# Kernel optimization log

Measured on AMD Instinct MI355X. Metric: run time of the kernel, lower is better.

## Reference

```python
import jax, jax.numpy as jnp
import numpy as np

POOL_NUM = 1024
NEIGHBOR_NUM = 16


def setup_inputs() -> dict:
    key = jax.random.key(0)
    k1, k2 = jax.random.split(key)
    vertices = jax.random.normal(k1, (8, 4096, 3), dtype=jnp.float32)
    feature_map = jax.random.normal(k2, (8, 4096, 256), dtype=jnp.float32)
    return {"vertices": vertices, "feature_map": feature_map}


def _get_neighbor_index(vertices, neighbor_num):
    # vertices: (bs, N, 3) -> neighbor_index: (bs, N, neighbor_num)
    inner = jnp.einsum('bnd,bmd->bnm', vertices, vertices)  # (bs, N, N)
    quadratic = jnp.sum(vertices ** 2, axis=2)              # (bs, N)
    distance = -2.0 * inner + quadratic[:, None, :] + quadratic[:, :, None]
    # smallest k+1 distances -> top_k on negated distance
    _, idx = jax.lax.top_k(-distance, neighbor_num + 1)     # (bs, N, k+1)
    return idx[:, :, 1:]                                    # drop self


def reference(vertices, feature_map):
    bs, vertice_num, _ = vertices.shape
    neighbor_index = _get_neighbor_index(vertices, NEIGHBOR_NUM)  # (bs, N, k)
    # gather neighbor features: (bs, N, k, C)
    id_0 = jnp.arange(bs)[:, None, None]
    neighbor_feature = feature_map[id_0, neighbor_index]
    pooled_feature = jnp.max(neighbor_feature, axis=2)            # (bs, N, C)
    # deterministic random subsample of vertices (torch uses randperm)
    sample_idx = jax.random.permutation(jax.random.key(42), vertice_num)[:POOL_NUM]
    vertices_pool = vertices[:, sample_idx, :]                    # (bs, P, 3)
    feature_map_pool = pooled_feature[:, sample_idx, :]           # (bs, P, C)
    return (vertices_pool, feature_map_pool)
```

## Files before the change

kernel.cpp:

```cpp
#include <hip/hip_runtime.h>
#include <stdint.h>
#include <string.h>
#include <algorithm>

#define NV 4096
#define NPOOL 1024
#define NB 8
#define KNB 16
#define REMOVED 0xFFFFFFFFu
#define HIDX(b) ((((b) >> 4) | (((b) & 15) << 6)))

struct SIdx { unsigned short v[NPOOL]; };

static inline void tf2x32_host(uint32_t k0, uint32_t k1,
                               uint32_t c0, uint32_t c1,
                               uint32_t& o0, uint32_t& o1) {
  uint32_t ks0 = k0, ks1 = k1, ks2 = k0 ^ k1 ^ 0x1BD11BDAu;
  uint32_t x0 = c0 + ks0, x1 = c1 + ks1;
#define TFR(r) { x0 += x1; x1 = (x1 << (r)) | (x1 >> (32 - (r))); x1 ^= x0; }
  TFR(13) TFR(15) TFR(26) TFR(6)
  x0 += ks1; x1 += ks2 + 1u;
  TFR(17) TFR(29) TFR(16) TFR(24)
  x0 += ks2; x1 += ks0 + 2u;
  TFR(13) TFR(15) TFR(26) TFR(6)
  x0 += ks0; x1 += ks1 + 3u;
  TFR(17) TFR(29) TFR(16) TFR(24)
  x0 += ks1; x1 += ks2 + 4u;
  TFR(13) TFR(15) TFR(26) TFR(6)
  x0 += ks2; x1 += ks0 + 5u;
#undef TFR
  o0 = x0; o1 = x1;
}

static void compute_sample_idx(SIdx& out) {
  static_assert(sizeof(SIdx) == 2048, "kernarg size");
  uint64_t arr[NV];
  uint16_t x[NV], tmp[NV];
  for (int i = 0; i < NV; ++i) x[i] = (uint16_t)i;
  uint32_t kh = 0u, kl = 42u;
  for (int round = 0; round < 2; ++round) {
    uint32_t nkh, nkl, sh, sl, t0, t1;
    tf2x32_host(kh, kl, 0u, 0u, nkh, nkl);
    tf2x32_host(kh, kl, 0u, 1u, sh, sl);
    kh = nkh; kl = nkl;
    for (int i = 0; i < NV; ++i) {
      tf2x32_host(sh, sl, 0u, (uint32_t)i, t0, t1);
      arr[i] = ((uint64_t)(t0 ^ t1) << 32) | (uint32_t)i;
    }
    std::sort(arr, arr + NV);
    for (int i = 0; i < NV; ++i) tmp[i] = x[(uint32_t)(arr[i] & 0xffffffffu)];
    memcpy(x, tmp, sizeof(x));
  }
  for (int i = 0; i < NPOOL; ++i) out.v[i] = x[i];
}

__global__ __launch_bounds__(256) void knn_pool_kernel(
    const float* __restrict__ vertices, const float* __restrict__ fm,
    const SIdx sidx,
    float* __restrict__ outV, float* __restrict__ outF) {
  __shared__ uint32_t hist[1024];
  __shared__ unsigned long long cand[64];
  __shared__ unsigned long long wmin[4];
  __shared__ int winners[KNB];
  __shared__ int s_ncand, s_taub;

  const int tid = threadIdx.x;
  const int lane = tid & 63;
  const int warp = tid >> 6;
  const int q = blockIdx.x;
  const int b = q & 7;
  const int i = q >> 3;
  const int n = (int)sidx.v[i];

  const float* vb = vertices + (size_t)b * NV * 3;
  const float qx = vb[n * 3 + 0], qy = vb[n * 3 + 1], qz = vb[n * 3 + 2];
  const float qn = __fadd_rn(__fadd_rn(__fmul_rn(qx, qx), __fmul_rn(qy, qy)),
                             __fmul_rn(qz, qz));

  const float4* vb4 = (const float4*)vb + tid * 12;
  float f[48];
#pragma unroll
  for (int j = 0; j < 12; ++j) {
    const float4 v4 = vb4[j];
    f[4 * j + 0] = v4.x; f[4 * j + 1] = v4.y;
    f[4 * j + 2] = v4.z; f[4 * j + 3] = v4.w;
  }

  uint32_t d[16];
#pragma unroll
  for (int t = 0; t < 16; ++t) {
    const int m = (tid << 4) + t;
    const float cx = f[3 * t + 0], cy = f[3 * t + 1], cz = f[3 * t + 2];
    const float inner = __fmaf_rn(cz, qz, __fmaf_rn(cy, qy, __fmul_rn(cx, qx)));
    const float qm = __fadd_rn(__fadd_rn(__fmul_rn(cx, cx), __fmul_rn(cy, cy)),
                               __fmul_rn(cz, cz));
    const float dist = __fadd_rn(__fadd_rn(__fmul_rn(-2.0f, inner), qm), qn);
    d[t] = (m == n) ? REMOVED : __float_as_uint(dist);
  }

  uint32_t mn = d[0];
#pragma unroll
  for (int t = 1; t < 16; ++t) mn = (d[t] < mn) ? d[t] : mn;

  hist[tid] = 0; hist[tid + 256] = 0; hist[tid + 512] = 0; hist[tid + 768] = 0;
  if (tid == 0) s_ncand = 0;
  __syncthreads();

  atomicAdd(&hist[HIDX(mn >> 22)], 1u);
  __syncthreads();

  if (warp == 0) {
    uint32_t s = 0;
#pragma unroll
    for (int j = 0; j < 16; ++j) s += hist[j * 64 + lane];
    uint32_t inc = s;
    for (int off = 1; off < 64; off <<= 1) {
      const uint32_t o = (uint32_t)__shfl_up((int)inc, off);
      if (lane >= off) inc += o;
    }
    const uint32_t pre = inc - s;
    const bool cross = (pre < KNB) && (inc >= KNB);
    const unsigned long long bal = __ballot(cross);
    const int leader = __ffsll((unsigned long long)bal) - 1;
    if (lane == leader) {
      uint32_t c = pre;
      int tb = lane * 16 + 15;
      for (int j = 0; j < 16; ++j) {
        const uint32_t h = hist[j * 64 + lane];
        if (c + h >= KNB) { tb = lane * 16 + j; break; }
        c += h;
      }
      s_taub = tb;
    }
  }
  __syncthreads();

  const uint32_t taub = (uint32_t)s_taub;

#pragma unroll
  for (int t = 0; t < 16; ++t) {
    const uint32_t v = d[t];
    if ((v >> 22) <= taub) {
      const int s = atomicAdd(&s_ncand, 1);
      if (s < 64)
        cand[s] = ((unsigned long long)v << 32) | (uint32_t)((tid << 4) + t);
    }
  }
  __syncthreads();

  const int C = s_ncand;
  if (C <= 64) {
    if (warp == 0) {
      const unsigned long long me =
          (lane < C) ? cand[lane] : 0xFFFFFFFFFFFFFFFFull;
      int rank = 0;
      for (int j = 0; j < C; ++j)
        rank += (cand[j] < me) ? 1 : 0;
      if (lane < C && rank < KNB) winners[rank] = (int)(me & 0xFFFFFFFFu);
    }
    __syncthreads();
  } else {
    uint32_t mask = 0;
    for (int r = 0; r < KNB; ++r) {
      uint32_t bv = REMOVED, bm = 0xFFFFFFFFu;
#pragma unroll
      for (int t = 0; t < 16; ++t) {
        const uint32_t v = (((mask >> t) & 1u) || ((d[t] >> 22) > taub))
                               ? REMOVED : d[t];
        const uint32_t m = (uint32_t)((tid << 4) + t);
        if (v < bv || (v == bv && m < bm)) { bv = v; bm = m; }
      }
      for (int off = 32; off > 0; off >>= 1) {
        const uint32_t ov = (uint32_t)__shfl_down((int)bv, off);
        const uint32_t om = (uint32_t)__shfl_down((int)bm, off);
        if (ov < bv || (ov == bv && om < bm)) { bv = ov; bm = om; }
      }
      if (lane == 0) wmin[warp] = ((unsigned long long)bv << 32) | bm;
      __syncthreads();
      const unsigned long long p0 = wmin[0], p1 = wmin[1];
      const unsigned long long p2 = wmin[2], p3 = wmin[3];
      const unsigned long long pa = (p0 < p1) ? p0 : p1;
      const unsigned long long pb = (p2 < p3) ? p2 : p3;
      const int w = (int)(((pa < pb) ? pa : pb) & 0xFFFFFFFFu);
      if (tid == 0) winners[r] = w;
      if (tid == (w >> 4)) mask |= 1u << (w & 15);
      __syncthreads();
    }
  }

  const float* fmb = fm + (size_t)b * NV * 256;
  float af = -INFINITY;
#pragma unroll
  for (int s = 0; s < KNB; ++s) {
    const int w = winners[s];
    af = fmaxf(af, fmb[(size_t)w * 256 + tid]);
  }
  outF[((size_t)b * NPOOL + i) * 256 + tid] = af;

  if (tid < 3) {
    outV[((size_t)b * NPOOL + i) * 3 + tid] = vb[n * 3 + tid];
  }
}

extern "C" void kernel_launch(void* const* d_in, const int* in_sizes, int n_in,
                              void* d_out, int out_size, void* d_ws, size_t ws_size,
                              hipStream_t stream) {
  const float* vertices = (const float*)d_in[0];
  const float* fm = (const float*)d_in[1];
  float* out = (float*)d_out;
  float* outV = out;
  float* outF = out + NB * NPOOL * 3;

  SIdx sidx;
  compute_sample_idx(sidx);

  knn_pool_kernel<<<NB * NPOOL, 256, 0, stream>>>(vertices, fm, sidx, outV, outF);
}
```

Measured before the change: 40.96 us.

## Process two query points per block to reuse loaded candidate vertices

Each block now handles two sampled query vertices instead of one, so the 4096 candidate coordinates loaded into registers serve two distance computations. Histograms, candidate lists and winner arrays are duplicated, and the two selection passes run in separate warps. The feature max-gather is vectorized with float4 loads over two warps. The grid is halved, which reduces parallelism and adds register pressure from keeping two distance arrays live.

```diff
diff --git a/kernel.cpp b/kernel.cpp
--- a/kernel.cpp
+++ b/kernel.cpp
@@ -54,28 +54,63 @@
   for (int i = 0; i < NPOOL; ++i) out.v[i] = x[i];
 }
 
+#define FALLBACK(D, TAUB, WIN)                                             \
+  {                                                                        \
+    uint32_t mask = 0;                                                     \
+    for (int r = 0; r < KNB; ++r) {                                        \
+      uint32_t bv = REMOVED, bm = 0xFFFFFFFFu;                             \
+      _Pragma("unroll")                                                    \
+      for (int t = 0; t < 16; ++t) {                                       \
+        const uint32_t v = (((mask >> t) & 1u) || ((D[t] >> 22) > (TAUB))) \
+                               ? REMOVED : D[t];                           \
+        const uint32_t m = (uint32_t)((tid << 4) + t);                     \
+        if (v < bv || (v == bv && m < bm)) { bv = v; bm = m; }             \
+      }                                                                    \
+      for (int off = 32; off > 0; off >>= 1) {                             \
+        const uint32_t ov = (uint32_t)__shfl_down((int)bv, off);           \
+        const uint32_t om = (uint32_t)__shfl_down((int)bm, off);           \
+        if (ov < bv || (ov == bv && om < bm)) { bv = ov; bm = om; }        \
+      }                                                                    \
+      if (lane == 0) wmin[warp] = ((unsigned long long)bv << 32) | bm;     \
+      __syncthreads();                                                     \
+      const unsigned long long p0 = wmin[0], p1 = wmin[1];                 \
+      const unsigned long long p2 = wmin[2], p3 = wmin[3];                 \
+      const unsigned long long pa = (p0 < p1) ? p0 : p1;                   \
+      const unsigned long long pb = (p2 < p3) ? p2 : p3;                   \
+      const int w = (int)(((pa < pb) ? pa : pb) & 0xFFFFFFFFu);            \
+      if (tid == 0) (WIN)[r] = w;                                          \
+      if (tid == (w >> 4)) mask |= 1u << (w & 15);                         \
+      __syncthreads();                                                     \
+    }                                                                      \
+  }
+
 __global__ __launch_bounds__(256) void knn_pool_kernel(
     const float* __restrict__ vertices, const float* __restrict__ fm,
     const SIdx sidx,
     float* __restrict__ outV, float* __restrict__ outF) {
-  __shared__ uint32_t hist[1024];
-  __shared__ unsigned long long cand[64];
+  __shared__ uint32_t hist0[1024], hist1[1024];
+  __shared__ unsigned long long cand0[64], cand1[64];
   __shared__ unsigned long long wmin[4];
-  __shared__ int winners[KNB];
-  __shared__ int s_ncand, s_taub;
+  __shared__ int winners0[KNB], winners1[KNB];
+  __shared__ int s_nc0, s_nc1, s_tb0, s_tb1;
 
   const int tid = threadIdx.x;
   const int lane = tid & 63;
   const int warp = tid >> 6;
-  const int q = blockIdx.x;
-  const int b = q & 7;
-  const int i = q >> 3;
-  const int n = (int)sidx.v[i];
+  const int blk = blockIdx.x;
+  const int b = blk & 7;
+  const int i0 = (blk >> 3) << 1;
+  const int i1 = i0 | 1;
+  const int n0 = (int)sidx.v[i0];
+  const int n1 = (int)sidx.v[i1];
 
   const float* vb = vertices + (size_t)b * NV * 3;
-  const float qx = vb[n * 3 + 0], qy = vb[n * 3 + 1], qz = vb[n * 3 + 2];
-  const float qn = __fadd_rn(__fadd_rn(__fmul_rn(qx, qx), __fmul_rn(qy, qy)),
-                             __fmul_rn(qz, qz));
+  const float q0x = vb[n0 * 3 + 0], q0y = vb[n0 * 3 + 1], q0z = vb[n0 * 3 + 2];
+  const float q1x = vb[n1 * 3 + 0], q1y = vb[n1 * 3 + 1], q1z = vb[n1 * 3 + 2];
+  const float qn0 = __fadd_rn(__fadd_rn(__fmul_rn(q0x, q0x), __fmul_rn(q0y, q0y)),
+                              __fmul_rn(q0z, q0z));
+  const float qn1 = __fadd_rn(__fadd_rn(__fmul_rn(q1x, q1x), __fmul_rn(q1y, q1y)),
+                              __fmul_rn(q1z, q1z));
 
   const float4* vb4 = (const float4*)vb + tid * 12;
   float f[48];
@@ -86,33 +121,43 @@
     f[4 * j + 2] = v4.z; f[4 * j + 3] = v4.w;
   }
 
-  uint32_t d[16];
+  uint32_t d0[16], d1[16];
 #pragma unroll
   for (int t = 0; t < 16; ++t) {
     const int m = (tid << 4) + t;
     const float cx = f[3 * t + 0], cy = f[3 * t + 1], cz = f[3 * t + 2];
-    const float inner = __fmaf_rn(cz, qz, __fmaf_rn(cy, qy, __fmul_rn(cx, qx)));
     const float qm = __fadd_rn(__fadd_rn(__fmul_rn(cx, cx), __fmul_rn(cy, cy)),
                                __fmul_rn(cz, cz));
-    const float dist = __fadd_rn(__fadd_rn(__fmul_rn(-2.0f, inner), qm), qn);
-    d[t] = (m == n) ? REMOVED : __float_as_uint(dist);
-  }
-
-  uint32_t mn = d[0];
-#pragma unroll
-  for (int t = 1; t < 16; ++t) mn = (d[t] < mn) ? d[t] : mn;
-
-  hist[tid] = 0; hist[tid + 256] = 0; hist[tid + 512] = 0; hist[tid + 768] = 0;
-  if (tid == 0) s_ncand = 0;
-  __syncthreads();
-
-  atomicAdd(&hist[HIDX(mn >> 22)], 1u);
-  __syncthreads();
-
-  if (warp == 0) {
+    const float in0 = __fmaf_rn(cz, q0z, __fmaf_rn(cy, q0y, __fmul_rn(cx, q0x)));
+    const float in1 = __fmaf_rn(cz, q1z, __fmaf_rn(cy, q1y, __fmul_rn(cx, q1x)));
+    const float ds0 = __fadd_rn(__fadd_rn(__fmul_rn(-2.0f, in0), qm), qn0);
+    const float ds1 = __fadd_rn(__fadd_rn(__fmul_rn(-2.0f, in1), qm), qn1);
+    d0[t] = (m == n0) ? REMOVED : __float_as_uint(ds0);
+    d1[t] = (m == n1) ? REMOVED : __float_as_uint(ds1);
+  }
+
+  uint32_t mn0 = d0[0], mn1 = d1[0];
+#pragma unroll
+  for (int t = 1; t < 16; ++t) {
+    mn0 = (d0[t] < mn0) ? d0[t] : mn0;
+    mn1 = (d1[t] < mn1) ? d1[t] : mn1;
+  }
+
+  const uint4 z4 = make_uint4(0, 0, 0, 0);
+  ((uint4*)hist0)[tid] = z4;
+  ((uint4*)hist1)[tid] = z4;
+  if (tid == 0) { s_nc0 = 0; s_nc1 = 0; }
+  __syncthreads();
+
+  atomicAdd(&hist0[HIDX(mn0 >> 22)], 1u);
+  atomicAdd(&hist1[HIDX(mn1 >> 22)], 1u);
+  __syncthreads();
+
+  if (warp < 2) {
+    uint32_t* H = (warp == 0) ? hist0 : hist1;
     uint32_t s = 0;
 #pragma unroll
-    for (int j = 0; j < 16; ++j) s += hist[j * 64 + lane];
+    for (int j = 0; j < 16; ++j) s += H[j * 64 + lane];
     uint32_t inc = s;
     for (int off = 1; off < 64; off <<= 1) {
       const uint32_t o = (uint32_t)__shfl_up((int)inc, off);
@@ -126,80 +171,70 @@
       uint32_t c = pre;
       int tb = lane * 16 + 15;
       for (int j = 0; j < 16; ++j) {
-        const uint32_t h = hist[j * 64 + lane];
+        const uint32_t h = H[j * 64 + lane];
         if (c + h >= KNB) { tb = lane * 16 + j; break; }
         c += h;
       }
-      s_taub = tb;
-    }
-  }
-  __syncthreads();
-
-  const uint32_t taub = (uint32_t)s_taub;
+      if (warp == 0) s_tb0 = tb; else s_tb1 = tb;
+    }
+  }
+  __syncthreads();
+
+  const uint32_t taub0 = (uint32_t)s_tb0;
+  const uint32_t taub1 = (uint32_t)s_tb1;
 
 #pragma unroll
   for (int t = 0; t < 16; ++t) {
-    const uint32_t v = d[t];
-    if ((v >> 22) <= taub) {
-      const int s = atomicAdd(&s_ncand, 1);
+    const uint32_t v0 = d0[t];
+    if ((v0 >> 22) <= taub0) {
+      const int s = atomicAdd(&s_nc0, 1);
       if (s < 64)
-        cand[s] = ((unsigned long long)v << 32) | (uint32_t)((tid << 4) + t);
-    }
-  }
-  __syncthreads();
-
-  const int C = s_ncand;
-  if (C <= 64) {
-    if (warp == 0) {
-      const unsigned long long me =
-          (lane < C) ? cand[lane] : 0xFFFFFFFFFFFFFFFFull;
-      int rank = 0;
-      for (int j = 0; j < C; ++j)
-        rank += (cand[j] < me) ? 1 : 0;
-      if (lane < C && rank < KNB) winners[rank] = (int)(me & 0xFFFFFFFFu);
-    }
-    __syncthreads();
-  } else {
-    uint32_t mask = 0;
-    for (int r = 0; r < KNB; ++r) {
-      uint32_t bv = REMOVED, bm = 0xFFFFFFFFu;
-#pragma unroll
-      for (int t = 0; t < 16; ++t) {
-        const uint32_t v = (((mask >> t) & 1u) || ((d[t] >> 22) > taub))
-                               ? REMOVED : d[t];
-        const uint32_t m = (uint32_t)((tid << 4) + t);
-        if (v < bv || (v == bv && m < bm)) { bv = v; bm = m; }
-      }
-      for (int off = 32; off > 0; off >>= 1) {
-        const uint32_t ov = (uint32_t)__shfl_down((int)bv, off);
-        const uint32_t om = (uint32_t)__shfl_down((int)bm, off);
-        if (ov < bv || (ov == bv && om < bm)) { bv = ov; bm = om; }
-      }
-      if (lane == 0) wmin[warp] = ((unsigned long long)bv << 32) | bm;
-      __syncthreads();
-      const unsigned long long p0 = wmin[0], p1 = wmin[1];
-      const unsigned long long p2 = wmin[2], p3 = wmin[3];
-      const unsigned long long pa = (p0 < p1) ? p0 : p1;
-      const unsigned long long pb = (p2 < p3) ? p2 : p3;
-      const int w = (int)(((pa < pb) ? pa : pb) & 0xFFFFFFFFu);
-      if (tid == 0) winners[r] = w;
-      if (tid == (w >> 4)) mask |= 1u << (w & 15);
-      __syncthreads();
-    }
-  }
+        cand0[s] = ((unsigned long long)v0 << 32) | (uint32_t)((tid << 4) + t);
+    }
+    const uint32_t v1 = d1[t];
+    if ((v1 >> 22) <= taub1) {
+      const int s = atomicAdd(&s_nc1, 1);
+      if (s < 64)
+        cand1[s] = ((unsigned long long)v1 << 32) | (uint32_t)((tid << 4) + t);
+    }
+  }
+  __syncthreads();
+
+  const int C0 = s_nc0, C1 = s_nc1;
+  if (warp == 0 && C0 <= 64) {
+    const unsigned long long me =
+        (lane < C0) ? cand0[lane] : 0xFFFFFFFFFFFFFFFFull;
+    int rank = 0;
+    for (int j = 0; j < C0; ++j) rank += (cand0[j] < me) ? 1 : 0;
+    if (lane < C0 && rank < KNB) winners0[rank] = (int)(me & 0xFFFFFFFFu);
+  }
+  if (warp == 1 && C1 <= 64) {
+    const unsigned long long me =
+        (lane < C1) ? cand1[lane] : 0xFFFFFFFFFFFFFFFFull;
+    int rank = 0;
+    for (int j = 0; j < C1; ++j) rank += (cand1[j] < me) ? 1 : 0;
+    if (lane < C1 && rank < KNB) winners1[rank] = (int)(me & 0xFFFFFFFFu);
+  }
+  __syncthreads();
+
+  if (C0 > 64) FALLBACK(d0, taub0, winners0);
+  if (C1 > 64) FALLBACK(d1, taub1, winners1);
 
   const float* fmb = fm + (size_t)b * NV * 256;
-  float af = -INFINITY;
-#pragma unroll
-  for (int s = 0; s < KNB; ++s) {
-    const int w = winners[s];
-    af = fmaxf(af, fmb[(size_t)w * 256 + tid]);
-  }
-  outF[((size_t)b * NPOOL + i) * 256 + tid] = af;
-
-  if (tid < 3) {
-    outV[((size_t)b * NPOOL + i) * 3 + tid] = vb[n * 3 + tid];
-  }
+  if (warp < 2) {
+    const int* W = (warp == 0) ? winners0 : winners1;
+    const int ii = (warp == 0) ? i0 : i1;
+    float4 acc = make_float4(-INFINITY, -INFINITY, -INFINITY, -INFINITY);
+#pragma unroll
+    for (int s = 0; s < KNB; ++s) {
+      const float4 v = ((const float4*)(fmb + (size_t)W[s] * 256))[lane];
+      acc.x = fmaxf(acc.x, v.x); acc.y = fmaxf(acc.y, v.y);
+      acc.z = fmaxf(acc.z, v.z); acc.w = fmaxf(acc.w, v.w);
+    }
+    ((float4*)(outF + ((size_t)b * NPOOL + ii) * 256))[lane] = acc;
+  }
+  if (warp == 2 && lane < 3) outV[((size_t)b * NPOOL + i0) * 3 + lane] = vb[n0 * 3 + lane];
+  if (warp == 3 && lane < 3) outV[((size_t)b * NPOOL + i1) * 3 + lane] = vb[n1 * 3 + lane];
 }
 
 extern "C" void kernel_launch(void* const* d_in, const int* in_sizes, int n_in,
@@ -214,5 +249,5 @@
   SIdx sidx;
   compute_sample_idx(sidx);
 
-  knn_pool_kernel<<<NB * NPOOL, 256, 0, stream>>>(vertices, fm, sidx, outV, outF);
-}
+  knn_pool_kernel<<<NB * NPOOL / 2, 256, 0, stream>>>(vertices, fm, sidx, outV, outF);
+}
```

Result: faster. 36.11 us, median of 2 (-11.9%).

## Use single-wavefront blocks with recomputed distances and float4 feature gather

Applied to the files above, without the earlier changes.

Shrinks each query block from 256 threads to one 64-lane wavefront, so each lane covers 64 candidate vertices. Distances are recomputed in two passes (histogram min, then candidate collection) instead of being held in registers, and the fallback top-k runs without cross-warp shared-memory reductions or block barriers. The feature max-gather uses float4 loads per lane, and the candidate buffer grows to 128 entries. This removes inter-warp synchronisation and register pressure, at the cost of redundant distance arithmetic and vertex reloads, plus a coarser per-lane histogram minimum that may admit more candidates.

```diff
diff --git a/kernel.cpp b/kernel.cpp
--- a/kernel.cpp
+++ b/kernel.cpp
@@ -8,6 +8,7 @@
 #define NB 8
 #define KNB 16
 #define REMOVED 0xFFFFFFFFu
+#define CANDCAP 128
 #define HIDX(b) ((((b) >> 4) | (((b) & 15) << 6)))
 
 struct SIdx { unsigned short v[NPOOL]; };
@@ -54,22 +55,38 @@
   for (int i = 0; i < NPOOL; ++i) out.v[i] = x[i];
 }
 
-__global__ __launch_bounds__(256) void knn_pool_kernel(
+__device__ __forceinline__ void dist4(const float4* __restrict__ vb4, int g,
+                                      float qx, float qy, float qz, float qn,
+                                      int selfT, uint32_t dv[4]) {
+  const float4 A = vb4[g * 3 + 0];
+  const float4 B = vb4[g * 3 + 1];
+  const float4 Cc = vb4[g * 3 + 2];
+  const float xs[12] = {A.x, A.y, A.z, A.w, B.x, B.y, B.z, B.w,
+                        Cc.x, Cc.y, Cc.z, Cc.w};
+#pragma unroll
+  for (int k = 0; k < 4; ++k) {
+    const float cx = xs[3 * k + 0], cy = xs[3 * k + 1], cz = xs[3 * k + 2];
+    const float inner = __fmaf_rn(cz, qz, __fmaf_rn(cy, qy, __fmul_rn(cx, qx)));
+    const float qm = __fadd_rn(__fadd_rn(__fmul_rn(cx, cx), __fmul_rn(cy, cy)),
+                               __fmul_rn(cz, cz));
+    const float ds = __fadd_rn(__fadd_rn(__fmul_rn(-2.0f, inner), qm), qn);
+    dv[k] = ((g * 4 + k) == selfT) ? REMOVED : __float_as_uint(ds);
+  }
+}
+
+__global__ __launch_bounds__(64) void knn_pool_kernel(
     const float* __restrict__ vertices, const float* __restrict__ fm,
     const SIdx sidx,
     float* __restrict__ outV, float* __restrict__ outF) {
   __shared__ uint32_t hist[1024];
-  __shared__ unsigned long long cand[64];
-  __shared__ unsigned long long wmin[4];
+  __shared__ unsigned long long cand[CANDCAP];
   __shared__ int winners[KNB];
-  __shared__ int s_ncand, s_taub;
-
-  const int tid = threadIdx.x;
-  const int lane = tid & 63;
-  const int warp = tid >> 6;
-  const int q = blockIdx.x;
-  const int b = q & 7;
-  const int i = q >> 3;
+  __shared__ int s_nc, s_tb;
+
+  const int lane = threadIdx.x;
+  const int blk = blockIdx.x;
+  const int b = blk & 7;
+  const int i = blk >> 3;
   const int n = (int)sidx.v[i];
 
   const float* vb = vertices + (size_t)b * NV * 3;
@@ -77,39 +94,30 @@
   const float qn = __fadd_rn(__fadd_rn(__fmul_rn(qx, qx), __fmul_rn(qy, qy)),
                              __fmul_rn(qz, qz));
 
-  const float4* vb4 = (const float4*)vb + tid * 12;
-  float f[48];
-#pragma unroll
-  for (int j = 0; j < 12; ++j) {
-    const float4 v4 = vb4[j];
-    f[4 * j + 0] = v4.x; f[4 * j + 1] = v4.y;
-    f[4 * j + 2] = v4.z; f[4 * j + 3] = v4.w;
-  }
-
-  uint32_t d[16];
-#pragma unroll
-  for (int t = 0; t < 16; ++t) {
-    const int m = (tid << 4) + t;
-    const float cx = f[3 * t + 0], cy = f[3 * t + 1], cz = f[3 * t + 2];
-    const float inner = __fmaf_rn(cz, qz, __fmaf_rn(cy, qy, __fmul_rn(cx, qx)));
-    const float qm = __fadd_rn(__fadd_rn(__fmul_rn(cx, cx), __fmul_rn(cy, cy)),
-                               __fmul_rn(cz, cz));
-    const float dist = __fadd_rn(__fadd_rn(__fmul_rn(-2.0f, inner), qm), qn);
-    d[t] = (m == n) ? REMOVED : __float_as_uint(dist);
-  }
-
-  uint32_t mn = d[0];
-#pragma unroll
-  for (int t = 1; t < 16; ++t) mn = (d[t] < mn) ? d[t] : mn;
-
-  hist[tid] = 0; hist[tid + 256] = 0; hist[tid + 512] = 0; hist[tid + 768] = 0;
-  if (tid == 0) s_ncand = 0;
+  const int selfT = ((n >> 6) == lane) ? (n & 63) : -1;
+  const float4* vb4 = (const float4*)vb + lane * 48;
+
+  {
+    const uint4 z4 = make_uint4(0, 0, 0, 0);
+    uint4* h4 = (uint4*)hist;
+    h4[lane] = z4; h4[lane + 64] = z4; h4[lane + 128] = z4; h4[lane + 192] = z4;
+  }
+  if (lane == 0) s_nc = 0;
+
+  uint32_t mn = REMOVED;
+#pragma unroll 4
+  for (int g = 0; g < 16; ++g) {
+    uint32_t dv[4];
+    dist4(vb4, g, qx, qy, qz, qn, selfT, dv);
+#pragma unroll
+    for (int k = 0; k < 4; ++k) mn = (dv[k] < mn) ? dv[k] : mn;
+  }
   __syncthreads();
 
   atomicAdd(&hist[HIDX(mn >> 22)], 1u);
   __syncthreads();
 
-  if (warp == 0) {
+  {
     uint32_t s = 0;
 #pragma unroll
     for (int j = 0; j < 16; ++j) s += hist[j * 64 + lane];
@@ -130,76 +138,84 @@
         if (c + h >= KNB) { tb = lane * 16 + j; break; }
         c += h;
       }
-      s_taub = tb;
-    }
-  }
-  __syncthreads();
-
-  const uint32_t taub = (uint32_t)s_taub;
-
-#pragma unroll
-  for (int t = 0; t < 16; ++t) {
-    const uint32_t v = d[t];
-    if ((v >> 22) <= taub) {
-      const int s = atomicAdd(&s_ncand, 1);
-      if (s < 64)
-        cand[s] = ((unsigned long long)v << 32) | (uint32_t)((tid << 4) + t);
-    }
-  }
-  __syncthreads();
-
-  const int C = s_ncand;
-  if (C <= 64) {
-    if (warp == 0) {
-      const unsigned long long me =
-          (lane < C) ? cand[lane] : 0xFFFFFFFFFFFFFFFFull;
-      int rank = 0;
-      for (int j = 0; j < C; ++j)
-        rank += (cand[j] < me) ? 1 : 0;
-      if (lane < C && rank < KNB) winners[rank] = (int)(me & 0xFFFFFFFFu);
-    }
+      s_tb = tb;
+    }
+  }
+  __syncthreads();
+  const uint32_t taub = (uint32_t)s_tb;
+
+#pragma unroll 4
+  for (int g = 0; g < 16; ++g) {
+    uint32_t dv[4];
+    dist4(vb4, g, qx, qy, qz, qn, selfT, dv);
+#pragma unroll
+    for (int k = 0; k < 4; ++k) {
+      const uint32_t v = dv[k];
+      if ((v >> 22) <= taub) {
+        const int s = atomicAdd(&s_nc, 1);
+        if (s < CANDCAP)
+          cand[s] = ((unsigned long long)v << 32) |
+                    (uint32_t)((lane << 6) + g * 4 + k);
+      }
+    }
+  }
+  __syncthreads();
+
+  const int C = s_nc;
+  if (C <= CANDCAP) {
+    const unsigned long long me0 =
+        (lane < C) ? cand[lane] : 0xFFFFFFFFFFFFFFFFull;
+    const unsigned long long me1 =
+        (lane + 64 < C) ? cand[lane + 64] : 0xFFFFFFFFFFFFFFFFull;
+    int r0 = 0, r1 = 0;
+    for (int j = 0; j < C; ++j) {
+      const unsigned long long cj = cand[j];
+      r0 += (cj < me0) ? 1 : 0;
+      r1 += (cj < me1) ? 1 : 0;
+    }
+    if (lane < C && r0 < KNB) winners[r0] = (int)(me0 & 0xFFFFFFFFu);
+    if (lane + 64 < C && r1 < KNB) winners[r1] = (int)(me1 & 0xFFFFFFFFu);
     __syncthreads();
   } else {
-    uint32_t mask = 0;
+    unsigned long long mask = 0ull;
     for (int r = 0; r < KNB; ++r) {
       uint32_t bv = REMOVED, bm = 0xFFFFFFFFu;
-#pragma unroll
-      for (int t = 0; t < 16; ++t) {
-        const uint32_t v = (((mask >> t) & 1u) || ((d[t] >> 22) > taub))
-                               ? REMOVED : d[t];
-        const uint32_t m = (uint32_t)((tid << 4) + t);
-        if (v < bv || (v == bv && m < bm)) { bv = v; bm = m; }
+#pragma unroll 2
+      for (int g = 0; g < 16; ++g) {
+        uint32_t dv[4];
+        dist4(vb4, g, qx, qy, qz, qn, selfT, dv);
+#pragma unroll
+        for (int k = 0; k < 4; ++k) {
+          const int t = g * 4 + k;
+          uint32_t v = dv[k];
+          if (((mask >> t) & 1ull) || ((v >> 22) > taub)) v = REMOVED;
+          const uint32_t m = (uint32_t)((lane << 6) + t);
+          if (v < bv || (v == bv && m < bm)) { bv = v; bm = m; }
+        }
       }
       for (int off = 32; off > 0; off >>= 1) {
         const uint32_t ov = (uint32_t)__shfl_down((int)bv, off);
         const uint32_t om = (uint32_t)__shfl_down((int)bm, off);
         if (ov < bv || (ov == bv && om < bm)) { bv = ov; bm = om; }
       }
-      if (lane == 0) wmin[warp] = ((unsigned long long)bv << 32) | bm;
-      __syncthreads();
-      const unsigned long long p0 = wmin[0], p1 = wmin[1];
-      const unsigned long long p2 = wmin[2], p3 = wmin[3];
-      const unsigned long long pa = (p0 < p1) ? p0 : p1;
-      const unsigned long long pb = (p2 < p3) ? p2 : p3;
-      const int w = (int)(((pa < pb) ? pa : pb) & 0xFFFFFFFFu);
-      if (tid == 0) winners[r] = w;
-      if (tid == (w >> 4)) mask |= 1u << (w & 15);
-      __syncthreads();
-    }
+      const int w = __shfl((int)bm, 0);
+      if (lane == 0) winners[r] = w;
+      if (lane == (w >> 6)) mask |= 1ull << (w & 63);
+    }
+    __syncthreads();
   }
 
   const float* fmb = fm + (size_t)b * NV * 256;
-  float af = -INFINITY;
-#pragma unroll
-  for (int s = 0; s < KNB; ++s) {
-    const int w = winners[s];
-    af = fmaxf(af, fmb[(size_t)w * 256 + tid]);
-  }
-  outF[((size_t)b * NPOOL + i) * 256 + tid] = af;
-
-  if (tid < 3) {
-    outV[((size_t)b * NPOOL + i) * 3 + tid] = vb[n * 3 + tid];
-  }
+  float4 acc = make_float4(-INFINITY, -INFINITY, -INFINITY, -INFINITY);
+#pragma unroll
+  for (int s2 = 0; s2 < KNB; ++s2) {
+    const int w = winners[s2];
+    const float4 v = ((const float4*)(fmb + (size_t)w * 256))[lane];
+    acc.x = fmaxf(acc.x, v.x); acc.y = fmaxf(acc.y, v.y);
+    acc.z = fmaxf(acc.z, v.z); acc.w = fmaxf(acc.w, v.w);
+  }
+  ((float4*)(outF + ((size_t)b * NPOOL + i) * 256))[lane] = acc;
+  if (lane < 3) outV[((size_t)b * NPOOL + i) * 3 + lane] = vb[n * 3 + lane];
 }
 
 extern "C" void kernel_launch(void* const* d_in, const int* in_sizes, int n_in,
@@ -214,5 +230,5 @@
   SIdx sidx;
   compute_sample_idx(sidx);
 
-  knn_pool_kernel<<<NB * NPOOL, 256, 0, stream>>>(vertices, fm, sidx, outV, outF);
-}
+  knn_pool_kernel<<<NB * NPOOL, 64, 0, stream>>>(vertices, fm, sidx, outV, outF);
+}
```

After: 111.1 us. +171.2%, slower.
